# Kernel optimization log

Measured on AMD Instinct MI355X. Metric: run time of the kernel, lower is better.

Reference implementation:

```python
import jax, jax.numpy as jnp
import numpy as np

HID = 512      # hidden_dim
MID = 256      # hid_dim
COND_D = 256   # condition_op_dim
OP_D = 32      # operator_len
EX_D = 32      # extra_info_num
L, N, T = 16, 1024, 8
EPS = 1e-5


def _lstm_cell(x_proj, h, c, Whh, bhh):
    # x_proj: precomputed x @ Wih.T + bih, shape [B, 4H]
    gates = x_proj + h @ Whh.T + bhh
    i, f, g, o = jnp.split(gates, 4, axis=-1)
    i = jax.nn.sigmoid(i); f = jax.nn.sigmoid(f)
    g = jnp.tanh(g); o = jax.nn.sigmoid(o)
    c = f * c + i * g
    h = o * jnp.tanh(c)
    return h, c


def _batchnorm(x, gamma, beta):
    mu = x.mean(0)
    var = x.var(0)  # biased, matches PyTorch training-mode normalization
    return gamma * (x - mu) * jax.lax.rsqrt(var + EPS) + beta


def setup_inputs() -> dict:
    key = jax.random.key(0)
    ks = jax.random.split(key, 24)
    s = lambda *sh: 0.05
    inp = {
        'operators': jax.random.normal(ks[0], (L, N, OP_D), jnp.float32),
        'extra_infos': jax.random.normal(ks[1], (L, N, EX_D), jnp.float32),
        'conditions': jax.random.normal(ks[2], (L, N, T, COND_D), jnp.float32),
        'condition_masks': jnp.ones((L, N, 1), jnp.float32),
        'mapping': jax.random.randint(ks[3], (L, N, 2), 0, N + 1, jnp.int32).astype(jnp.int64),
        'lstm1_Wih': jax.random.normal(ks[4], (4 * HID, COND_D), jnp.float32) * 0.05,
        'lstm1_Whh': jax.random.normal(ks[5], (4 * HID, HID), jnp.float32) * 0.05,
        'lstm1_bih': jnp.zeros((4 * HID,), jnp.float32),
        'lstm1_bhh': jnp.zeros((4 * HID,), jnp.float32),
        'cond_W': jax.random.normal(ks[6], (MID, HID), jnp.float32) * 0.05,
        'cond_b': jnp.zeros((MID,), jnp.float32),
        'bn1_g': jnp.ones((MID,), jnp.float32),
        'bn1_b': jnp.zeros((MID,), jnp.float32),
        'lstm2_Wih': jax.random.normal(ks[7], (4 * HID, OP_D + EX_D + MID), jnp.float32) * 0.05,
        'lstm2_Whh': jax.random.normal(ks[8], (4 * HID, HID), jnp.float32) * 0.05,
        'lstm2_bih': jnp.zeros((4 * HID,), jnp.float32),
        'lstm2_bhh': jnp.zeros((4 * HID,), jnp.float32),
        'bn2_g': jnp.ones((HID,), jnp.float32),
        'bn2_b': jnp.zeros((HID,), jnp.float32),
    }
    return inp


def reference(operators, extra_infos, conditions, condition_masks, mapping,
              lstm1_Wih, lstm1_Whh, lstm1_bih, lstm1_bhh,
              cond_W, cond_b, bn1_g, bn1_b,
              lstm2_Wih, lstm2_Whh, lstm2_bih, lstm2_bhh,
              bn2_g, bn2_b):
    B = L * N
    x = conditions.reshape(B, T, COND_D)
    # lstm1 over conditions; precompute input projections for all steps
    xp = jnp.einsum('btd,gd->btg', x, lstm1_Wih) + lstm1_bih  # [B,T,4H]

    def step1(carry, xt):
        h, c = carry
        h, c = _lstm_cell(xt, h, c, lstm1_Whh, lstm1_bhh)
        return (h, c), None

    h0 = jnp.zeros((B, HID), xp.dtype)
    (h1, _), _ = jax.lax.scan(step1, (h0, h0), jnp.swapaxes(xp, 0, 1))

    last = jax.nn.relu(h1 @ cond_W.T + cond_b)       # [B, MID]
    last = _batchnorm(last, bn1_g, bn1_b).reshape(L, N, MID)

    out = jnp.concatenate([operators, extra_infos, last], axis=2)  # [L,N,IN2]
    xp2 = jnp.einsum('lnd,gd->lng', out, lstm2_Wih) + lstm2_bih    # [L,N,4H]

    hz = jnp.zeros((N, HID), xp2.dtype)
    h, c = _lstm_cell(xp2[L - 1], hz, hz, lstm2_Whh, lstm2_bhh)

    mapping = mapping.astype(jnp.int32)
    levels = jnp.arange(L - 2, -1, -1)

    def tree_step(carry, idx):
        h, c = carry
        mp = mapping[idx]  # [N,2]
        pad = jnp.zeros((1, HID), h.dtype)
        ph = jnp.concatenate([pad, h], 0)  # [N+1,H]
        pc = jnp.concatenate([pad, c], 0)
        h = (ph[mp[:, 0]] + ph[mp[:, 1]]) * 0.5
        c = (pc[mp[:, 0]] + pc[mp[:, 1]]) * 0.5
        h, c = _lstm_cell(xp2[idx], h, c, lstm2_Whh, lstm2_bhh)
        return (h, c), None

    (h, c), _ = jax.lax.scan(tree_step, (h, c), levels)

    # batch_size == N since all operator rows are nonzero
    return _batchnorm(h, bn2_g, bn2_b)  # [N, HID]
```

## Files before the change

kernel.cpp:

```cpp
#include <hip/hip_runtime.h>
#include <hip/hip_bf16.h>
#include <stdint.h>


typedef __bf16 bf16;
typedef __bf16 bf16x8 __attribute__((ext_vector_type(8)));
typedef float f32x4 __attribute__((ext_vector_type(4)));

#define HIDDEN 512

__device__ __forceinline__ float fast_sig(float x) { return 1.f / (1.f + __expf(-x)); }
__device__ __forceinline__ float fast_tanh(float x) {
  float e = __expf(2.f * x);
  return 1.f - 2.f / (e + 1.f);
}

__device__ __forceinline__ void async16(const bf16* g, bf16* l) {
  __builtin_amdgcn_global_load_lds(
      (const __attribute__((address_space(1))) void*)g,
      (__attribute__((address_space(3))) void*)l, 16, 0, 0);
}

__device__ __forceinline__ void cvt_one(const float* __restrict__ src,
                                        bf16* __restrict__ dst, size_t i) {
  float4 a = *(const float4*)(src + i);
  float4 b = *(const float4*)(src + i + 4);
  bf16x8 r;
  r[0] = (bf16)a.x; r[1] = (bf16)a.y; r[2] = (bf16)a.z; r[3] = (bf16)a.w;
  r[4] = (bf16)b.x; r[5] = (bf16)b.y; r[6] = (bf16)b.z; r[7] = (bf16)b.w;
  *(bf16x8*)(dst + i) = r;
}

__global__ void prep(const float* conds, bf16* conds_b,
                     const float* s0, bf16* d0, const float* s1, bf16* d1,
                     const float* s2, bf16* d2, const float* s3, bf16* d3,
                     const float* s4, bf16* d4, const float* s5, bf16* d5,
                     const float* s6, bf16* d6,
                     const int* map, int* flags) {
  int b = blockIdx.x;
  int tid = threadIdx.x;
  if (b < 2176) {
    int g = b * 256 + tid;
    const float* s; bf16* d; int off;
    if      (g < 65536)  { s = s0; d = d0; off = g; }
    else if (g < 131072) { s = s1; d = d1; off = g - 65536; }
    else if (g < 196608) { s = s2; d = d2; off = g - 131072; }
    else if (g < 327680) { s = s3; d = d3; off = g - 196608; }
    else if (g < 344064) { s = s4; d = d4; off = g - 327680; }
    else if (g < 425984) { s = s5; d = d5; off = g - 344064; }
    else if (g < 557056) { s = s6; d = d6; off = g - 425984; }
    else return;
    cvt_one(s, d, (size_t)off * 8);
  } else if (b == 2176) {
    __shared__ int any;
    if (tid == 0) any = 0;
    __syncthreads();
    int loc = 0;
    for (int i = tid; i < 16384; i += 256) loc |= map[2 * i + 1];
    if (loc) atomicOr(&any, 1);
    __syncthreads();
    if (tid == 0) flags[0] = (any == 0) ? 1 : 0;
  } else {
    size_t i = ((size_t)(b - 2177) * 256 + tid) * 8;
    cvt_one(conds, conds_b, i);
  }
}

template <int KT0, int KT1>
__global__ __launch_bounds__(256, 2) void cell_gemm_w(
    const bf16* __restrict__ A0, int a0off, int a0s,
    const bf16* __restrict__ A1, int a1s,
    const bf16* __restrict__ B0, int b0s,
    const bf16* __restrict__ B1, int b1s,
    const float* __restrict__ bias0, const float* __restrict__ bias1,
    const float* __restrict__ c_prev,
    float* __restrict__ c_out,
    bf16* __restrict__ h_b16)
{
  __shared__ __align__(16) bf16 sA[128 * 64];
  __shared__ __align__(16) bf16 sB[256 * 64];
  const int tid = threadIdx.x;
  const int lane = tid & 63;
  const int quad = lane >> 4, cl = lane & 15;
  const int wave = tid >> 6;
  const int wr = wave >> 1, wc = wave & 1;
  const int bm0 = blockIdx.x * 128;
  const int j0 = blockIdx.y * 64;

  const bf16* ra[4][2];
  const bf16* rb[8][2];
#pragma unroll
  for (int mi = 0; mi < 4; ++mi)
#pragma unroll
    for (int kh = 0; kh < 2; ++kh) {
      int row = wr * 64 + mi * 16 + cl;
      ra[mi][kh] = &sA[row * 64 + (((kh * 4 + quad) ^ (row & 7))) * 8];
    }
#pragma unroll
  for (int ni = 0; ni < 8; ++ni)
#pragma unroll
    for (int kh = 0; kh < 2; ++kh) {
      int row = (ni & 3) * 64 + wc * 32 + (ni >> 2) * 16 + cl;
      rb[ni][kh] = &sB[row * 64 + (((kh * 4 + quad) ^ (row & 7))) * 8];
    }

  f32x4 acc[4][8];
#pragma unroll
  for (int mi = 0; mi < 4; ++mi)
#pragma unroll
    for (int ni = 0; ni < 8; ++ni) acc[mi][ni] = f32x4{0.f, 0.f, 0.f, 0.f};

  const bf16* pa[4];
  const bf16* pb[8];
#pragma unroll
  for (int ia = 0; ia < 4; ++ia) {
    int e = ia * 256 + tid, row = e >> 3, sl = e & 7;
    pa[ia] = A0 + (size_t)((bm0 + row) * a0s + a0off + (sl ^ (row & 7)) * 8);
  }
#pragma unroll
  for (int ib = 0; ib < 8; ++ib) {
    int e = ib * 256 + tid, row = e >> 3, sl = e & 7;
    int wrow = (row >> 6) * HIDDEN + j0 + (row & 63);
    pb[ib] = B0 + (size_t)(wrow * b0s + (sl ^ (row & 7)) * 8);
  }

  auto ktile = [&]() {
#pragma unroll
    for (int ia = 0; ia < 4; ++ia) {
      async16(pa[ia], sA + (ia * 256 + tid) * 8);
      pa[ia] += 64;
    }
#pragma unroll
    for (int ib = 0; ib < 8; ++ib) {
      async16(pb[ib], sB + (ib * 256 + tid) * 8);
      pb[ib] += 64;
    }
    __syncthreads();
#pragma unroll
    for (int kh = 0; kh < 2; ++kh) {
      bf16x8 af[4], bfr[8];
#pragma unroll
      for (int mi = 0; mi < 4; ++mi) af[mi] = *(const bf16x8*)ra[mi][kh];
#pragma unroll
      for (int ni = 0; ni < 8; ++ni) bfr[ni] = *(const bf16x8*)rb[ni][kh];
#pragma unroll
      for (int mi = 0; mi < 4; ++mi)
#pragma unroll
        for (int ni = 0; ni < 8; ++ni)
          acc[mi][ni] = __builtin_amdgcn_mfma_f32_16x16x32_bf16(af[mi], bfr[ni], acc[mi][ni], 0, 0, 0);
    }
    __syncthreads();
  };

  for (int kt = 0; kt < KT0; ++kt) ktile();
  if (KT1 > 0) {
#pragma unroll
    for (int ia = 0; ia < 4; ++ia) {
      int e = ia * 256 + tid, row = e >> 3, sl = e & 7;
      pa[ia] = A1 + (size_t)((bm0 + row) * a1s + (sl ^ (row & 7)) * 8);
    }
#pragma unroll
    for (int ib = 0; ib < 8; ++ib) {
      int e = ib * 256 + tid, row = e >> 3, sl = e & 7;
      int wrow = (row >> 6) * HIDDEN + j0 + (row & 63);
      pb[ib] = B1 + (size_t)(wrow * b1s + (sl ^ (row & 7)) * 8);
    }
    for (int kt = 0; kt < KT1; ++kt) ktile();
  }

#pragma unroll
  for (int jq = 0; jq < 2; ++jq) {
    const int j = j0 + wc * 32 + jq * 16 + cl;
    float bI = bias0[j] + bias1[j];
    float bF = bias0[HIDDEN + j] + bias1[HIDDEN + j];
    float bG = bias0[2 * HIDDEN + j] + bias1[2 * HIDDEN + j];
    float bO = bias0[3 * HIDDEN + j] + bias1[3 * HIDDEN + j];
#pragma unroll
    for (int mi = 0; mi < 4; ++mi) {
      int rb_ = bm0 + wr * 64 + mi * 16 + quad * 4;
#pragma unroll
      for (int r = 0; r < 4; ++r) {
        int row = rb_ + r;
        float iv = fast_sig(acc[mi][0 + 4 * jq][r] + bI);
        float fv = fast_sig(acc[mi][1 + 4 * jq][r] + bF);
        float gv = fast_tanh(acc[mi][2 + 4 * jq][r] + bG);
        float ov = fast_sig(acc[mi][3 + 4 * jq][r] + bO);
        float cp = c_prev ? c_prev[(size_t)row * HIDDEN + j] : 0.f;
        float cn = fv * cp + iv * gv;
        float hn = ov * fast_tanh(cn);
        c_out[(size_t)row * HIDDEN + j] = cn;
        h_b16[(size_t)row * HIDDEN + j] = (bf16)hn;
      }
    }
  }
}

__global__ __launch_bounds__(256, 2) void cell_tree(
    const bf16* __restrict__ hA,
    const bf16* __restrict__ W,
    const float* __restrict__ bhh,
    const void* __restrict__ xp, int xpf,
    const float* __restrict__ c_prev,
    float* __restrict__ c_out,
    bf16* __restrict__ h_out,
    float* __restrict__ h_f32)
{
  __shared__ __align__(16) bf16 sA[32 * 64];
  __shared__ __align__(16) bf16 sB[128 * 64];
  const int tid = threadIdx.x;
  const int lane = tid & 63;
  const int quad = lane >> 4, cl = lane & 15;
  const int wave = tid >> 6;
  const int wr = wave >> 1, wc = wave & 1;
  const int bm0 = blockIdx.x * 32;
  const int j0 = blockIdx.y * 32;

  const bf16* ra[2];
  const bf16* rb[4][2];
#pragma unroll
  for (int kh = 0; kh < 2; ++kh) {
    int row = wr * 16 + cl;
    ra[kh] = &sA[row * 64 + (((kh * 4 + quad) ^ (row & 7))) * 8];
  }
#pragma unroll
  for (int g = 0; g < 4; ++g)
#pragma unroll
    for (int kh = 0; kh < 2; ++kh) {
      int row = g * 32 + wc * 16 + cl;
      rb[g][kh] = &sB[row * 64 + (((kh * 4 + quad) ^ (row & 7))) * 8];
    }

  f32x4 acc[4];
#pragma unroll
  for (int g = 0; g < 4; ++g) acc[g] = f32x4{0.f, 0.f, 0.f, 0.f};

  int row_a = tid >> 3, sl_a = tid & 7;
  const bf16* pa = hA + (size_t)((bm0 + row_a) * HIDDEN + (sl_a ^ (row_a & 7)) * 8);
  const bf16* pb[4];
#pragma unroll
  for (int ib = 0; ib < 4; ++ib) {
    int e = ib * 256 + tid, row = e >> 3, sl = e & 7;
    int wrow = (row >> 5) * HIDDEN + j0 + (row & 31);
    pb[ib] = W + (size_t)(wrow * HIDDEN + (sl ^ (row & 7)) * 8);
  }

  for (int kt = 0; kt < 8; ++kt) {
    async16(pa, sA + tid * 8);
    pa += 64;
#pragma unroll
    for (int ib = 0; ib < 4; ++ib) {
      async16(pb[ib], sB + (ib * 256 + tid) * 8);
      pb[ib] += 64;
    }
    __syncthreads();
#pragma unroll
    for (int kh = 0; kh < 2; ++kh) {
      bf16x8 af = *(const bf16x8*)ra[kh];
#pragma unroll
      for (int g = 0; g < 4; ++g) {
        bf16x8 bfr = *(const bf16x8*)rb[g][kh];
        acc[g] = __builtin_amdgcn_mfma_f32_16x16x32_bf16(af, bfr, acc[g], 0, 0, 0);
      }
    }
    __syncthreads();
  }

  const int j = j0 + wc * 16 + cl;
  float bI = bhh[j], bF = bhh[HIDDEN + j];
  float bG = bhh[2 * HIDDEN + j], bO = bhh[3 * HIDDEN + j];
  int rb0 = bm0 + wr * 16 + quad * 4;
#pragma unroll
  for (int r = 0; r < 4; ++r) {
    int row = rb0 + r;
    float gi = acc[0][r] + bI;
    float gf = acc[1][r] + bF;
    float gg = acc[2][r] + bG;
    float go = acc[3][r] + bO;
    size_t base = (size_t)row * 2048;
    if (xpf) {
      const float* xr = (const float*)xp + base;
      gi += xr[j]; gf += xr[HIDDEN + j];
      gg += xr[2 * HIDDEN + j]; go += xr[3 * HIDDEN + j];
    } else {
      const bf16* xr = (const bf16*)xp + base;
      gi += (float)xr[j]; gf += (float)xr[HIDDEN + j];
      gg += (float)xr[2 * HIDDEN + j]; go += (float)xr[3 * HIDDEN + j];
    }
    float cp = c_prev[(size_t)row * HIDDEN + j];
    float cn = fast_sig(gf) * cp + fast_sig(gi) * fast_tanh(gg);
    float hn = fast_sig(go) * fast_tanh(cn);
    c_out[(size_t)row * HIDDEN + j] = cn;
    h_out[(size_t)row * HIDDEN + j] = (bf16)hn;
    if (h_f32) h_f32[(size_t)row * HIDDEN + j] = hn;
  }
}

template <int MT>
__global__ __launch_bounds__(256, 2) void plain_gemm(
    const bf16* __restrict__ A0, int a0s, int a0kt,
    const bf16* __restrict__ A1, int a1s, int a1kt,
    const bf16* __restrict__ A2, int a2s, int a2kt,
    const bf16* __restrict__ B, int bs,
    const float* __restrict__ bias, int do_relu,
    bf16* __restrict__ outh, float* __restrict__ outf, int Ntot)
{
  constexpr int BM = MT * 32;
  __shared__ __align__(16) bf16 sA[BM * 32];
  __shared__ __align__(16) bf16 sB[128 * 32];
  const int tid = threadIdx.x;
  const int lane = tid & 63;
  const int quad = lane >> 4, cl = lane & 15;
  const int wave = tid >> 6;
  const int wr = wave >> 1, wc = wave & 1;
  const int bm0 = blockIdx.x * BM;
  const int bn0 = blockIdx.y * 128;

  f32x4 acc[MT][4];
#pragma unroll
  for (int mi = 0; mi < MT; ++mi)
#pragma unroll
    for (int ni = 0; ni < 4; ++ni) acc[mi][ni] = f32x4{0.f, 0.f, 0.f, 0.f};

  const int nkt = a0kt + a1kt + a2kt;
  for (int kt = 0; kt < nkt; ++kt) {
    const bf16* abase; int astr, acol;
    if (kt < a0kt)            { abase = A0; astr = a0s; acol = kt * 32; }
    else if (kt < a0kt + a1kt){ abase = A1; astr = a1s; acol = (kt - a0kt) * 32; }
    else                      { abase = A2; astr = a2s; acol = (kt - a0kt - a1kt) * 32; }
#pragma unroll
    for (int ia = 0; ia < MT / 2; ++ia) {
      int e = ia * 256 + tid;
      int row = e >> 2, sl = e & 3;
      int src = sl ^ ((row >> 1) & 3);
      async16(abase + (size_t)(bm0 + row) * astr + acol + src * 8, sA + e * 8);
    }
#pragma unroll
    for (int ib = 0; ib < 2; ++ib) {
      int e = ib * 256 + tid;
      int row = e >> 2, sl = e & 3;
      int src = sl ^ ((row >> 1) & 3);
      async16(B + (size_t)(bn0 + row) * bs + kt * 32 + src * 8, sB + e * 8);
    }
    __syncthreads();
    bf16x8 af[MT], bfr[4];
#pragma unroll
    for (int mi = 0; mi < MT; ++mi) {
      int row = wr * (MT * 16) + mi * 16 + cl;
      int sl = quad ^ ((row >> 1) & 3);
      af[mi] = *(const bf16x8*)&sA[row * 32 + sl * 8];
    }
#pragma unroll
    for (int ni = 0; ni < 4; ++ni) {
      int row = wc * 64 + ni * 16 + cl;
      int sl = quad ^ ((row >> 1) & 3);
      bfr[ni] = *(const bf16x8*)&sB[row * 32 + sl * 8];
    }
#pragma unroll
    for (int mi = 0; mi < MT; ++mi)
#pragma unroll
      for (int ni = 0; ni < 4; ++ni)
        acc[mi][ni] = __builtin_amdgcn_mfma_f32_16x16x32_bf16(af[mi], bfr[ni], acc[mi][ni], 0, 0, 0);
    __syncthreads();
  }

#pragma unroll
  for (int mi = 0; mi < MT; ++mi) {
    int rb = bm0 + wr * (MT * 16) + mi * 16 + quad * 4;
#pragma unroll
    for (int ni = 0; ni < 4; ++ni) {
      int col = bn0 + wc * 64 + ni * 16 + cl;
      float bv = bias ? bias[col] : 0.f;
#pragma unroll
      for (int r = 0; r < 4; ++r) {
        int row = rb + r;
        float v = acc[mi][ni][r] + bv;
        if (do_relu) v = fmaxf(v, 0.f);
        if (outf) outf[(size_t)row * Ntot + col] = v;
        else      outh[(size_t)row * Ntot + col] = (bf16)v;
      }
    }
  }
}

__global__ void gather_h(const int* __restrict__ map, const int* __restrict__ flags,
                         int level,
                         const bf16* __restrict__ h_src, const float* __restrict__ c_src,
                         bf16* __restrict__ hA, float* __restrict__ c_dst)
{
  int n = blockIdx.x, t = threadIdx.x;
  long base = (long)level * 2048 + n * 2;
  int m0, m1;
  if (flags[0]) { m0 = map[base * 2]; m1 = map[base * 2 + 2]; }
  else          { m0 = map[base];     m1 = map[base + 1]; }
  float h0 = m0 ? (float)h_src[(size_t)(m0 - 1) * HIDDEN + t] : 0.f;
  float h1 = m1 ? (float)h_src[(size_t)(m1 - 1) * HIDDEN + t] : 0.f;
  float c0 = m0 ? c_src[(size_t)(m0 - 1) * HIDDEN + t] : 0.f;
  float c1 = m1 ? c_src[(size_t)(m1 - 1) * HIDDEN + t] : 0.f;
  hA[(size_t)n * HIDDEN + t] = (bf16)(0.5f * (h0 + h1));
  c_dst[(size_t)n * HIDDEN + t] = 0.5f * (c0 + c1);
}

__global__ void cell0(const void* __restrict__ xp, int xp_f32,
                      const float* __restrict__ bhh,
                      bf16* __restrict__ h, float* __restrict__ c)
{
  int n = blockIdx.x, j = threadIdx.x;
  float g[4];
#pragma unroll
  for (int k = 0; k < 4; ++k) {
    size_t idx = (size_t)n * 2048 + k * 512 + j;
    float v = xp_f32 ? ((const float*)xp)[idx] : (float)((const bf16*)xp)[idx];
    g[k] = v + bhh[k * 512 + j];
  }
  float cv = fast_sig(g[0]) * fast_tanh(g[2]);
  h[(size_t)n * HIDDEN + j] = (bf16)(fast_sig(g[3]) * fast_tanh(cv));
  c[(size_t)n * HIDDEN + j] = cv;
}

__global__ void bn_reduce_b16(const bf16* __restrict__ x, int rpb, int F,
                              float* __restrict__ partials) {
  int col = threadIdx.x, b = blockIdx.x;
  const bf16* p = x + (size_t)b * rpb * F + col;
  float s = 0.f, q = 0.f;
  for (int r = 0; r < rpb; ++r) { float v = (float)p[(size_t)r * F]; s += v; q += v * v; }
  partials[(size_t)b * 2 * F + col] = s;
  partials[(size_t)b * 2 * F + F + col] = q;
}

__global__ void bn_reduce_f32(const float* __restrict__ x, int rpb, int F,
                              float* __restrict__ partials) {
  int col = threadIdx.x, b = blockIdx.x;
  const float* p = x + (size_t)b * rpb * F + col;
  float s = 0.f, q = 0.f;
  for (int r = 0; r < rpb; ++r) { float v = p[(size_t)r * F]; s += v; q += v * v; }
  partials[(size_t)b * 2 * F + col] = s;
  partials[(size_t)b * 2 * F + F + col] = q;
}

__global__ void bn_final(const float* __restrict__ partials, int nb, int F,
                         const float* __restrict__ g, const float* __restrict__ b,
                         float invB, float* __restrict__ scale, float* __restrict__ shift) {
  int j = threadIdx.x;
  float s = 0.f, q = 0.f;
  for (int i = 0; i < nb; ++i) {
    s += partials[(size_t)i * 2 * F + j];
    q += partials[(size_t)i * 2 * F + F + j];
  }
  float mu = s * invB;
  float var = fmaxf(q * invB - mu * mu, 0.f);
  float sc = g[j] * rsqrtf(var + 1e-5f);
  scale[j] = sc;
  shift[j] = b[j] - sc * mu;
}

__global__ void bn_apply_mid(const bf16* __restrict__ x, const float* __restrict__ scale,
                             const float* __restrict__ shift, int Fmask, size_t total,
                             bf16* __restrict__ out) {
  for (size_t i = blockIdx.x * (size_t)blockDim.x + threadIdx.x; i < total;
       i += (size_t)gridDim.x * blockDim.x) {
    int j = (int)(i & (size_t)Fmask);
    out[i] = (bf16)(scale[j] * (float)x[i] + shift[j]);
  }
}

__global__ void bn_apply_out(const float* __restrict__ x, const float* __restrict__ scale,
                             const float* __restrict__ shift, int Fmask, size_t total,
                             float* __restrict__ out) {
  for (size_t i = blockIdx.x * (size_t)blockDim.x + threadIdx.x; i < total;
       i += (size_t)gridDim.x * blockDim.x) {
    int j = (int)(i & (size_t)Fmask);
    out[i] = scale[j] * x[i] + shift[j];
  }
}

extern "C" void kernel_launch(void* const* d_in, const int* in_sizes, int n_in,
                              void* d_out, int out_size, void* d_ws, size_t ws_size,
                              hipStream_t stream) {
  const float* operators = (const float*)d_in[0];
  const float* extras    = (const float*)d_in[1];
  const float* conds     = (const float*)d_in[2];
  const int*   mapping   = (const int*)d_in[4];
  const float* b1ih = (const float*)d_in[7];
  const float* b1hh = (const float*)d_in[8];
  const float* condb = (const float*)d_in[10];
  const float* bn1g = (const float*)d_in[11];
  const float* bn1b = (const float*)d_in[12];
  const float* b2ih = (const float*)d_in[15];
  const float* b2hh = (const float*)d_in[16];
  const float* bn2g = (const float*)d_in[17];
  const float* bn2b = (const float*)d_in[18];

  char* ws = (char*)d_ws;
  size_t o = 0;
  auto alloc = [&](size_t bytes) {
    char* p = ws + o;
    o += (bytes + 255) & ~(size_t)255;
    return p;
  };
  bf16* conds_b = (bf16*)alloc((size_t)33554432 * 2);
  bf16* ops_b   = (bf16*)alloc((size_t)524288 * 2);
  bf16* ext_b   = (bf16*)alloc((size_t)524288 * 2);
  bf16* w1ih_b  = (bf16*)alloc((size_t)524288 * 2);
  bf16* w1hh_b  = (bf16*)alloc((size_t)1048576 * 2);
  bf16* condw_b = (bf16*)alloc((size_t)131072 * 2);
  bf16* w2ih_b  = (bf16*)alloc((size_t)655360 * 2);
  bf16* w2hh_b  = (bf16*)alloc((size_t)1048576 * 2);
  bf16* h1[2];
  h1[0] = (bf16*)alloc((size_t)16384 * 512 * 2);
  h1[1] = (bf16*)alloc((size_t)16384 * 512 * 2);
  float* c1 = (float*)alloc((size_t)16384 * 512 * 4);
  bf16* last_relu = (bf16*)alloc((size_t)16384 * 256 * 2);
  bf16* last_bn = (bf16*)alloc((size_t)16384 * 256 * 2);
  bf16* h2 = (bf16*)alloc((size_t)1024 * 512 * 2);
  bf16* hA = (bf16*)alloc((size_t)1024 * 512 * 2);
  float* c2a = (float*)alloc((size_t)1024 * 512 * 4);
  float* c2b = (float*)alloc((size_t)1024 * 512 * 4);
  float* h2f = (float*)alloc((size_t)1024 * 512 * 4);
  float* partials = (float*)alloc((size_t)64 * 1024 * 4);
  float* scale1 = (float*)alloc(256 * 4);
  float* shift1 = (float*)alloc(256 * 4);
  float* scale2 = (float*)alloc(512 * 4);
  float* shift2 = (float*)alloc(512 * 4);
  int* flags = (int*)alloc(256);

  size_t xp2_elems = (size_t)16384 * 2048;
  int xpf = (o + xp2_elems * 4 <= ws_size) ? 1 : 0;
  void* xp2 = alloc(xp2_elems * (xpf ? 4 : 2));
  float* xp2f = xpf ? (float*)xp2 : nullptr;
  bf16* xp2h = xpf ? nullptr : (bf16*)xp2;

  prep<<<18561, 256, 0, stream>>>(
      conds, conds_b,
      operators, ops_b, extras, ext_b,
      (const float*)d_in[5], w1ih_b, (const float*)d_in[6], w1hh_b,
      (const float*)d_in[9], condw_b, (const float*)d_in[13], w2ih_b,
      (const float*)d_in[14], w2hh_b,
      mapping, flags);

  cell_gemm_w<4, 0><<<dim3(128, 8), 256, 0, stream>>>(
      conds_b, 0, 2048, nullptr, 512,
      w1ih_b, 256, w1hh_b, 512,
      b1ih, b1hh, nullptr, c1, h1[1]);
  for (int t = 1; t < 8; ++t) {
    cell_gemm_w<4, 8><<<dim3(128, 8), 256, 0, stream>>>(
        conds_b, t * 256, 2048, h1[t & 1], 512,
        w1ih_b, 256, w1hh_b, 512,
        b1ih, b1hh, c1, c1, h1[(t + 1) & 1]);
  }

  plain_gemm<2><<<dim3(256, 2), 256, 0, stream>>>(
      h1[0], 512, 16, nullptr, 0, 0, nullptr, 0, 0,
      condw_b, 512, condb, 1, last_relu, nullptr, 256);
  bn_reduce_b16<<<64, 256, 0, stream>>>(last_relu, 256, 256, partials);
  bn_final<<<1, 256, 0, stream>>>(partials, 64, 256, bn1g, bn1b, 1.f / 16384.f, scale1, shift1);
  bn_apply_mid<<<1024, 256, 0, stream>>>(last_relu, scale1, shift1, 255,
                                         (size_t)16384 * 256, last_bn);

  plain_gemm<4><<<dim3(128, 16), 256, 0, stream>>>(
      ops_b, 32, 1, ext_b, 32, 1, last_bn, 256, 8,
      w2ih_b, 320, b2ih, 0, xp2h, xp2f, 2048);

  size_t lvl_sz = (size_t)1024 * 2048;
  const void* xp15 = xpf ? (const void*)(xp2f + 15 * lvl_sz) : (const void*)(xp2h + 15 * lvl_sz);
  cell0<<<1024, 512, 0, stream>>>(xp15, xpf, b2hh, h2, c2a);
  for (int idx = 14; idx >= 0; --idx) {
    gather_h<<<1024, 512, 0, stream>>>(mapping, flags, idx, h2, c2a, hA, c2b);
    const void* xpl = xpf ? (const void*)(xp2f + idx * lvl_sz) : (const void*)(xp2h + idx * lvl_sz);
    cell_tree<<<dim3(32, 16), 256, 0, stream>>>(
        hA, w2hh_b, b2hh, xpl, xpf, c2b, c2a, h2,
        (idx == 0) ? h2f : nullptr);
  }

  bn_reduce_f32<<<16, 512, 0, stream>>>(h2f, 64, 512, partials);
  bn_final<<<1, 512, 0, stream>>>(partials, 16, 512, bn2g, bn2b, 1.f / 1024.f, scale2, shift2);
  bn_apply_out<<<512, 256, 0, stream>>>(h2f, scale2, shift2, 511,
                                        (size_t)1024 * 512, (float*)d_out);
}
```

Baseline: 1.167 ms.

## Shrink LSTM1 GEMM tile to 128x32 and store gate projections only in bf16

The LSTM1 cell GEMM tile is reduced from 128 rows x 64 hidden units (256 gate columns) to 128 rows x 32 hidden units (128 gate columns), doubling the grid to 2048 blocks. This lowers per-thread accumulator and register use and LDS footprint, and should allow higher occupancy and better CU fill, at the cost of re-reading the A tile twice as often. Separately, the xp2 gate-projection buffer is now always bf16 instead of fp32 when workspace allows, halving its write and read traffic. The bf16 storage adds some rounding error to the tree LSTM inputs.

```diff
diff --git a/kernel.cpp b/kernel.cpp
--- a/kernel.cpp
+++ b/kernel.cpp
@@ -66,8 +66,8 @@
   }
 }
 
-template <int KT0, int KT1>
-__global__ __launch_bounds__(256, 2) void cell_gemm_w(
+template <int MT, int KT0, int KT1>
+__global__ __launch_bounds__(256, 2) void cell_gemm(
     const bf16* __restrict__ A0, int a0off, int a0s,
     const bf16* __restrict__ A1, int a1s,
     const bf16* __restrict__ B0, int b0s,
@@ -77,77 +77,78 @@
     float* __restrict__ c_out,
     bf16* __restrict__ h_b16)
 {
-  __shared__ __align__(16) bf16 sA[128 * 64];
-  __shared__ __align__(16) bf16 sB[256 * 64];
+  constexpr int BM = MT * 32;
+  __shared__ __align__(16) bf16 sA[BM * 64];
+  __shared__ __align__(16) bf16 sB[128 * 64];
   const int tid = threadIdx.x;
   const int lane = tid & 63;
   const int quad = lane >> 4, cl = lane & 15;
   const int wave = tid >> 6;
   const int wr = wave >> 1, wc = wave & 1;
-  const int bm0 = blockIdx.x * 128;
-  const int j0 = blockIdx.y * 64;
-
-  const bf16* ra[4][2];
-  const bf16* rb[8][2];
-#pragma unroll
-  for (int mi = 0; mi < 4; ++mi)
+  const int bm0 = blockIdx.x * BM;
+  const int j0 = blockIdx.y * 32;
+
+  const bf16* ra[MT][2];
+  const bf16* rb[4][2];
+#pragma unroll
+  for (int mi = 0; mi < MT; ++mi)
 #pragma unroll
     for (int kh = 0; kh < 2; ++kh) {
-      int row = wr * 64 + mi * 16 + cl;
+      int row = wr * (MT * 16) + mi * 16 + cl;
       ra[mi][kh] = &sA[row * 64 + (((kh * 4 + quad) ^ (row & 7))) * 8];
     }
 #pragma unroll
-  for (int ni = 0; ni < 8; ++ni)
+  for (int g = 0; g < 4; ++g)
 #pragma unroll
     for (int kh = 0; kh < 2; ++kh) {
-      int row = (ni & 3) * 64 + wc * 32 + (ni >> 2) * 16 + cl;
-      rb[ni][kh] = &sB[row * 64 + (((kh * 4 + quad) ^ (row & 7))) * 8];
-    }
-
-  f32x4 acc[4][8];
-#pragma unroll
-  for (int mi = 0; mi < 4; ++mi)
-#pragma unroll
-    for (int ni = 0; ni < 8; ++ni) acc[mi][ni] = f32x4{0.f, 0.f, 0.f, 0.f};
-
-  const bf16* pa[4];
-  const bf16* pb[8];
-#pragma unroll
-  for (int ia = 0; ia < 4; ++ia) {
+      int row = g * 32 + wc * 16 + cl;
+      rb[g][kh] = &sB[row * 64 + (((kh * 4 + quad) ^ (row & 7))) * 8];
+    }
+
+  f32x4 acc[MT][4];
+#pragma unroll
+  for (int mi = 0; mi < MT; ++mi)
+#pragma unroll
+    for (int g = 0; g < 4; ++g) acc[mi][g] = f32x4{0.f, 0.f, 0.f, 0.f};
+
+  const bf16* pa[MT];
+  const bf16* pb[4];
+#pragma unroll
+  for (int ia = 0; ia < MT; ++ia) {
     int e = ia * 256 + tid, row = e >> 3, sl = e & 7;
     pa[ia] = A0 + (size_t)((bm0 + row) * a0s + a0off + (sl ^ (row & 7)) * 8);
   }
 #pragma unroll
-  for (int ib = 0; ib < 8; ++ib) {
+  for (int ib = 0; ib < 4; ++ib) {
     int e = ib * 256 + tid, row = e >> 3, sl = e & 7;
-    int wrow = (row >> 6) * HIDDEN + j0 + (row & 63);
+    int wrow = (row >> 5) * HIDDEN + j0 + (row & 31);
     pb[ib] = B0 + (size_t)(wrow * b0s + (sl ^ (row & 7)) * 8);
   }
 
   auto ktile = [&]() {
 #pragma unroll
-    for (int ia = 0; ia < 4; ++ia) {
+    for (int ia = 0; ia < MT; ++ia) {
       async16(pa[ia], sA + (ia * 256 + tid) * 8);
       pa[ia] += 64;
     }
 #pragma unroll
-    for (int ib = 0; ib < 8; ++ib) {
+    for (int ib = 0; ib < 4; ++ib) {
       async16(pb[ib], sB + (ib * 256 + tid) * 8);
       pb[ib] += 64;
     }
     __syncthreads();
 #pragma unroll
     for (int kh = 0; kh < 2; ++kh) {
-      bf16x8 af[4], bfr[8];
-#pragma unroll
-      for (int mi = 0; mi < 4; ++mi) af[mi] = *(const bf16x8*)ra[mi][kh];
-#pragma unroll
-      for (int ni = 0; ni < 8; ++ni) bfr[ni] = *(const bf16x8*)rb[ni][kh];
-#pragma unroll
-      for (int mi = 0; mi < 4; ++mi)
-#pragma unroll
-        for (int ni = 0; ni < 8; ++ni)
-          acc[mi][ni] = __builtin_amdgcn_mfma_f32_16x16x32_bf16(af[mi], bfr[ni], acc[mi][ni], 0, 0, 0);
+      bf16x8 af[MT], bfr[4];
+#pragma unroll
+      for (int mi = 0; mi < MT; ++mi) af[mi] = *(const bf16x8*)ra[mi][kh];
+#pragma unroll
+      for (int g = 0; g < 4; ++g) bfr[g] = *(const bf16x8*)rb[g][kh];
+#pragma unroll
+      for (int mi = 0; mi < MT; ++mi)
+#pragma unroll
+        for (int g = 0; g < 4; ++g)
+          acc[mi][g] = __builtin_amdgcn_mfma_f32_16x16x32_bf16(af[mi], bfr[g], acc[mi][g], 0, 0, 0);
     }
     __syncthreads();
   };
@@ -155,42 +156,39 @@
   for (int kt = 0; kt < KT0; ++kt) ktile();
   if (KT1 > 0) {
 #pragma unroll
-    for (int ia = 0; ia < 4; ++ia) {
+    for (int ia = 0; ia < MT; ++ia) {
       int e = ia * 256 + tid, row = e >> 3, sl = e & 7;
       pa[ia] = A1 + (size_t)((bm0 + row) * a1s + (sl ^ (row & 7)) * 8);
     }
 #pragma unroll
-    for (int ib = 0; ib < 8; ++ib) {
+    for (int ib = 0; ib < 4; ++ib) {
       int e = ib * 256 + tid, row = e >> 3, sl = e & 7;
-      int wrow = (row >> 6) * HIDDEN + j0 + (row & 63);
+      int wrow = (row >> 5) * HIDDEN + j0 + (row & 31);
       pb[ib] = B1 + (size_t)(wrow * b1s + (sl ^ (row & 7)) * 8);
     }
     for (int kt = 0; kt < KT1; ++kt) ktile();
   }
 
-#pragma unroll
-  for (int jq = 0; jq < 2; ++jq) {
-    const int j = j0 + wc * 32 + jq * 16 + cl;
-    float bI = bias0[j] + bias1[j];
-    float bF = bias0[HIDDEN + j] + bias1[HIDDEN + j];
-    float bG = bias0[2 * HIDDEN + j] + bias1[2 * HIDDEN + j];
-    float bO = bias0[3 * HIDDEN + j] + bias1[3 * HIDDEN + j];
-#pragma unroll
-    for (int mi = 0; mi < 4; ++mi) {
-      int rb_ = bm0 + wr * 64 + mi * 16 + quad * 4;
-#pragma unroll
-      for (int r = 0; r < 4; ++r) {
-        int row = rb_ + r;
-        float iv = fast_sig(acc[mi][0 + 4 * jq][r] + bI);
-        float fv = fast_sig(acc[mi][1 + 4 * jq][r] + bF);
-        float gv = fast_tanh(acc[mi][2 + 4 * jq][r] + bG);
-        float ov = fast_sig(acc[mi][3 + 4 * jq][r] + bO);
-        float cp = c_prev ? c_prev[(size_t)row * HIDDEN + j] : 0.f;
-        float cn = fv * cp + iv * gv;
-        float hn = ov * fast_tanh(cn);
-        c_out[(size_t)row * HIDDEN + j] = cn;
-        h_b16[(size_t)row * HIDDEN + j] = (bf16)hn;
-      }
+  const int j = j0 + wc * 16 + cl;
+  float bI = bias0[j] + bias1[j];
+  float bF = bias0[HIDDEN + j] + bias1[HIDDEN + j];
+  float bG = bias0[2 * HIDDEN + j] + bias1[2 * HIDDEN + j];
+  float bO = bias0[3 * HIDDEN + j] + bias1[3 * HIDDEN + j];
+#pragma unroll
+  for (int mi = 0; mi < MT; ++mi) {
+    int rb_ = bm0 + wr * (MT * 16) + mi * 16 + quad * 4;
+#pragma unroll
+    for (int r = 0; r < 4; ++r) {
+      int row = rb_ + r;
+      float iv = fast_sig(acc[mi][0][r] + bI);
+      float fv = fast_sig(acc[mi][1][r] + bF);
+      float gv = fast_tanh(acc[mi][2][r] + bG);
+      float ov = fast_sig(acc[mi][3][r] + bO);
+      float cp = c_prev ? c_prev[(size_t)row * HIDDEN + j] : 0.f;
+      float cn = fv * cp + iv * gv;
+      float hn = ov * fast_tanh(cn);
+      c_out[(size_t)row * HIDDEN + j] = cn;
+      h_b16[(size_t)row * HIDDEN + j] = (bf16)hn;
     }
   }
 }
@@ -199,7 +197,7 @@
     const bf16* __restrict__ hA,
     const bf16* __restrict__ W,
     const float* __restrict__ bhh,
-    const void* __restrict__ xp, int xpf,
+    const bf16* __restrict__ xp,
     const float* __restrict__ c_prev,
     float* __restrict__ c_out,
     bf16* __restrict__ h_out,
@@ -272,20 +270,11 @@
 #pragma unroll
   for (int r = 0; r < 4; ++r) {
     int row = rb0 + r;
-    float gi = acc[0][r] + bI;
-    float gf = acc[1][r] + bF;
-    float gg = acc[2][r] + bG;
-    float go = acc[3][r] + bO;
-    size_t base = (size_t)row * 2048;
-    if (xpf) {
-      const float* xr = (const float*)xp + base;
-      gi += xr[j]; gf += xr[HIDDEN + j];
-      gg += xr[2 * HIDDEN + j]; go += xr[3 * HIDDEN + j];
-    } else {
-      const bf16* xr = (const bf16*)xp + base;
-      gi += (float)xr[j]; gf += (float)xr[HIDDEN + j];
-      gg += (float)xr[2 * HIDDEN + j]; go += (float)xr[3 * HIDDEN + j];
-    }
+    const bf16* xr = xp + (size_t)row * 2048;
+    float gi = acc[0][r] + bI + (float)xr[j];
+    float gf = acc[1][r] + bF + (float)xr[HIDDEN + j];
+    float gg = acc[2][r] + bG + (float)xr[2 * HIDDEN + j];
+    float go = acc[3][r] + bO + (float)xr[3 * HIDDEN + j];
     float cp = c_prev[(size_t)row * HIDDEN + j];
     float cn = fast_sig(gf) * cp + fast_sig(gi) * fast_tanh(gg);
     float hn = fast_sig(go) * fast_tanh(cn);
@@ -302,7 +291,7 @@
     const bf16* __restrict__ A2, int a2s, int a2kt,
     const bf16* __restrict__ B, int bs,
     const float* __restrict__ bias, int do_relu,
-    bf16* __restrict__ outh, float* __restrict__ outf, int Ntot)
+    bf16* __restrict__ outh, int Ntot)
 {
   constexpr int BM = MT * 32;
   __shared__ __align__(16) bf16 sA[BM * 32];
@@ -375,8 +364,7 @@
         int row = rb + r;
         float v = acc[mi][ni][r] + bv;
         if (do_relu) v = fmaxf(v, 0.f);
-        if (outf) outf[(size_t)row * Ntot + col] = v;
-        else      outh[(size_t)row * Ntot + col] = (bf16)v;
+        outh[(size_t)row * Ntot + col] = (bf16)v;
       }
     }
   }
@@ -400,18 +388,15 @@
   c_dst[(size_t)n * HIDDEN + t] = 0.5f * (c0 + c1);
 }
 
-__global__ void cell0(const void* __restrict__ xp, int xp_f32,
+__global__ void cell0(const bf16* __restrict__ xp,
                       const float* __restrict__ bhh,
                       bf16* __restrict__ h, float* __restrict__ c)
 {
   int n = blockIdx.x, j = threadIdx.x;
   float g[4];
 #pragma unroll
-  for (int k = 0; k < 4; ++k) {
-    size_t idx = (size_t)n * 2048 + k * 512 + j;
-    float v = xp_f32 ? ((const float*)xp)[idx] : (float)((const bf16*)xp)[idx];
-    g[k] = v + bhh[k * 512 + j];
-  }
+  for (int k = 0; k < 4; ++k)
+    g[k] = (float)xp[(size_t)n * 2048 + k * 512 + j] + bhh[k * 512 + j];
   float cv = fast_sig(g[0]) * fast_tanh(g[2]);
   h[(size_t)n * HIDDEN + j] = (bf16)(fast_sig(g[3]) * fast_tanh(cv));
   c[(size_t)n * HIDDEN + j] = cv;
@@ -522,12 +507,7 @@
   float* scale2 = (float*)alloc(512 * 4);
   float* shift2 = (float*)alloc(512 * 4);
   int* flags = (int*)alloc(256);
-
-  size_t xp2_elems = (size_t)16384 * 2048;
-  int xpf = (o + xp2_elems * 4 <= ws_size) ? 1 : 0;
-  void* xp2 = alloc(xp2_elems * (xpf ? 4 : 2));
-  float* xp2f = xpf ? (float*)xp2 : nullptr;
-  bf16* xp2h = xpf ? nullptr : (bf16*)xp2;
+  bf16* xp2 = (bf16*)alloc((size_t)16384 * 2048 * 2);
 
   prep<<<18561, 256, 0, stream>>>(
       conds, conds_b,
@@ -537,12 +517,12 @@
       (const float*)d_in[14], w2hh_b,
       mapping, flags);
 
-  cell_gemm_w<4, 0><<<dim3(128, 8), 256, 0, stream>>>(
+  cell_gemm<4, 4, 0><<<dim3(128, 16), 256, 0, stream>>>(
       conds_b, 0, 2048, nullptr, 512,
       w1ih_b, 256, w1hh_b, 512,
       b1ih, b1hh, nullptr, c1, h1[1]);
   for (int t = 1; t < 8; ++t) {
-    cell_gemm_w<4, 8><<<dim3(128, 8), 256, 0, stream>>>(
+    cell_gemm<4, 4, 8><<<dim3(128, 16), 256, 0, stream>>>(
         conds_b, t * 256, 2048, h1[t & 1], 512,
         w1ih_b, 256, w1hh_b, 512,
         b1ih, b1hh, c1, c1, h1[(t + 1) & 1]);
@@ -550,7 +530,7 @@
 
   plain_gemm<2><<<dim3(256, 2), 256, 0, stream>>>(
       h1[0], 512, 16, nullptr, 0, 0, nullptr, 0, 0,
-      condw_b, 512, condb, 1, last_relu, nullptr, 256);
+      condw_b, 512, condb, 1, last_relu, 256);
   bn_reduce_b16<<<64, 256, 0, stream>>>(last_relu, 256, 256, partials);
   bn_final<<<1, 256, 0, stream>>>(partials, 64, 256, bn1g, bn1b, 1.f / 16384.f, scale1, shift1);
   bn_apply_mid<<<1024, 256, 0, stream>>>(last_relu, scale1, shift1, 255,
@@ -558,16 +538,14 @@
 
   plain_gemm<4><<<dim3(128, 16), 256, 0, stream>>>(
       ops_b, 32, 1, ext_b, 32, 1, last_bn, 256, 8,
-      w2ih_b, 320, b2ih, 0, xp2h, xp2f, 2048);
+      w2ih_b, 320, b2ih, 0, xp2, 2048);
 
   size_t lvl_sz = (size_t)1024 * 2048;
-  const void* xp15 = xpf ? (const void*)(xp2f + 15 * lvl_sz) : (const void*)(xp2h + 15 * lvl_sz);
-  cell0<<<1024, 512, 0, stream>>>(xp15, xpf, b2hh, h2, c2a);
+  cell0<<<1024, 512, 0, stream>>>(xp2 + 15 * lvl_sz, b2hh, h2, c2a);
   for (int idx = 14; idx >= 0; --idx) {
     gather_h<<<1024, 512, 0, stream>>>(mapping, flags, idx, h2, c2a, hA, c2b);
-    const void* xpl = xpf ? (const void*)(xp2f + idx * lvl_sz) : (const void*)(xp2h + idx * lvl_sz);
     cell_tree<<<dim3(32, 16), 256, 0, stream>>>(
-        hA, w2hh_b, b2hh, xpl, xpf, c2b, c2a, h2,
+        hA, w2hh_b, b2hh, xp2 + idx * lvl_sz, c2b, c2a, h2,
         (idx == 0) ? h2f : nullptr);
   }
 
```

Result: faster. 1.133 ms (-2.9%).
